# Kernel tuning notes

Measured on AMD Instinct MI355X. Metric: run time of the kernel, lower is better.

## Reference

```python
import jax, jax.numpy as jnp
import numpy as np

EMBED_DIM = 256
NUM_HEADS = 8
HEAD_DIM = EMBED_DIM // NUM_HEADS
SCALE = HEAD_DIM ** -0.5  # note: scale uses head_dim even though attention is over full D
EPS = 1e-12  # torch F.normalize eps


def setup_inputs() -> dict:
    key = jax.random.key(0)
    k1, k2, k3 = jax.random.split(key, 3)
    B, Nq, Nk, D = 4, 4096, 4096, EMBED_DIM
    return {
        "query": jax.random.normal(k1, (B, Nq, D), dtype=jnp.float32),
        "key": jax.random.normal(k2, (B, Nk, D), dtype=jnp.float32),
        "value": jax.random.normal(k3, (B, Nk, D), dtype=jnp.float32),
    }


def _l2_normalize(x):
    # matches torch.nn.functional.normalize(x, dim=-1): x / max(||x||, eps)
    n = jnp.linalg.norm(x, axis=-1, keepdims=True)
    return x / jnp.maximum(n, EPS)


def reference(query, key, value):
    q = _l2_normalize(query)          # (B, Nq, D)
    k = _l2_normalize(key)            # (B, Nk, D)
    scores = jnp.einsum("bqd,bkd->bqk", q, k) * SCALE  # (B, Nq, Nk) cosine sims
    attn = jax.nn.softmax(scores, axis=-1)
    return jnp.einsum("bqk,bkd->bqd", attn, value)     # (B, Nq, D)
```

## Files before the change

### kernel.cpp

```cpp
#include <hip/hip_runtime.h>


#define NQ 4096
#define NK 4096
#define DIM 256
#define NROWS 16384
#define BM 128
#define BN 64
#define KSPLIT 2
#define NITER 32

typedef __attribute__((ext_vector_type(8))) short bf16x8;
typedef __attribute__((ext_vector_type(4))) float f32x4;
typedef __attribute__((ext_vector_type(16))) float f32x16;

__device__ __forceinline__ unsigned short f2bf(float f) {
  unsigned int u = __float_as_uint(f);
  u += 0x7fffu + ((u >> 16) & 1u);
  return (unsigned short)(u >> 16);
}

__device__ __forceinline__ void gload16(const void* g, void* l) {
  __builtin_amdgcn_global_load_lds(
      (const __attribute__((address_space(1))) unsigned int*)g,
      (__attribute__((address_space(3))) unsigned int*)l, 16, 0, 0);
}

__global__ __launch_bounds__(256) void prep_qk(
    const float* __restrict__ Q, const float* __restrict__ K,
    unsigned short* __restrict__ Qfm, unsigned short* __restrict__ Kfm)
{
  const int wave = threadIdx.x >> 6, lane = threadIdx.x & 63;
  const int r = blockIdx.x * 4 + wave;
  const bool isQ = r < NROWS;
  const int R = isQ ? r : r - NROWS;
  const float* src = (isQ ? Q : K) + (size_t)R * DIM + lane * 4;
  float4 v = *(const float4*)src;
  float ss = v.x*v.x + v.y*v.y + v.z*v.z + v.w*v.w;
  #pragma unroll
  for (int off = 1; off < 64; off <<= 1) ss += __shfl_xor(ss, off, 64);
  float scale = 1.0f / fmaxf(sqrtf(ss), 1e-12f);
  if (isQ) scale *= (0.17677669529663687f * 1.4426950408889634f);
  unsigned short b0 = f2bf(v.x*scale), b1 = f2bf(v.y*scale),
                 b2 = f2bf(v.z*scale), b3 = f2bf(v.w*scale);
  ushort4 o; o.x = b0; o.y = b1; o.z = b2; o.w = b3;
  if (isQ) {
    const int mb = R >> 4, m = R & 15;
    const int kg = lane >> 3, fl = m + 16 * ((lane >> 1) & 3), j0 = 4 * (lane & 1);
    *(ushort4*)(Qfm + ((size_t)(mb*8 + kg)*64 + fl)*8 + j0) = o;
  } else {
    const int kt = R >> 6, n = R & 63;
    const int c = lane >> 1, j0 = 4 * (lane & 1);
    *(ushort4*)(Kfm + ((size_t)(kt*32 + c)*64 + n)*8 + j0) = o;
  }
}

__global__ __launch_bounds__(256) void prep_v(
    const float* __restrict__ V, unsigned short* __restrict__ Vfm)
{
  const int NS = blockIdx.x;
  const int t = threadIdx.x;
  #pragma unroll
  for (int i = 0; i < 4; i++) {
    const int e = t + 256*i;
    const int nl = e >> 6;
    const int d  = (e & 63) * 4;
    float4 v = *(const float4*)(V + ((size_t)NS*16 + nl)*DIM + d);
    const int db = d >> 5;
    const int lane = (d & 31) + 32*((nl >> 3) & 1);
    const int j = nl & 7;
    size_t base = ((size_t)(NS*8 + db)*64 + lane)*8 + j;
    Vfm[base]      = f2bf(v.x);
    Vfm[base + 8]  = f2bf(v.y);
    Vfm[base + 16] = f2bf(v.z);
    Vfm[base + 24] = f2bf(v.w);
  }
}

__global__ __launch_bounds__(512, 2) void attn(
    const unsigned short* __restrict__ Qfm,
    const unsigned short* __restrict__ Kfm,
    const unsigned short* __restrict__ Vfm,
    float* __restrict__ Opart, float* __restrict__ lpart)
{
  __shared__ unsigned short Klds[64 * 256];
  __shared__ unsigned short Plds[128 * 64];

  const int tid = threadIdx.x, wave = tid >> 6, lane = tid & 63;
  const int blk = blockIdx.x;
  const int g = blk & 7, qt = blk >> 3;
  const int b = g >> 1, ks = g & 1;
  const int Rq0 = b*NQ + qt*BM;
  const int MB0 = Rq0 >> 4;
  const int n0base = b*NQ + ks*(NK/KSPLIT);
  const int mi = wave >> 1, ni = wave & 1;
  const int mi2 = wave >> 2, dh = wave & 3;

  bf16x8 qf[2][8];
  #pragma unroll
  for (int mt = 0; mt < 2; mt++) {
    const int mb = MB0 + mi*2 + mt;
    #pragma unroll
    for (int kg = 0; kg < 8; kg++)
      qf[mt][kg] = *(const bf16x8*)(Qfm + ((size_t)(mb*8 + kg)*64 + lane)*8);
  }

  f32x16 oacc[2][2] = {};
  float lacc[2][4] = {};

  auto stage = [&](int kt) {
    const int ktile = (n0base + kt*BN) >> 6;
    #pragma unroll
    for (int jj = 0; jj < 4; jj++) {
      const int c = wave*4 + jj;
      gload16(Kfm + ((size_t)(ktile*32 + c)*64 + lane)*8, Klds + (size_t)c*512);
    }
  };

  stage(0);

  for (int kt = 0; kt < NITER; kt++) {
    __syncthreads();

    f32x4 sacc[2][2] = {};
    #pragma unroll
    for (int kg = 0; kg < 8; kg++) {
      bf16x8 kf[2];
      #pragma unroll
      for (int nt = 0; nt < 2; nt++) {
        const int nrow = ni*32 + nt*16 + (lane & 15);
        const int c = kg*4 + (lane >> 4);
        kf[nt] = *(const bf16x8*)(Klds + ((size_t)(c*64 + nrow))*8);
      }
      #pragma unroll
      for (int mt = 0; mt < 2; mt++)
        #pragma unroll
        for (int nt = 0; nt < 2; nt++)
          sacc[mt][nt] = __builtin_amdgcn_mfma_f32_16x16x32_bf16(
              qf[mt][kg], kf[nt], sacc[mt][nt], 0, 0, 0);
    }

    #pragma unroll
    for (int mt = 0; mt < 2; mt++)
      #pragma unroll
      for (int nt = 0; nt < 2; nt++)
        #pragma unroll
        for (int r = 0; r < 4; r++) {
          float p = __builtin_amdgcn_exp2f(sacc[mt][nt][r]);
          lacc[mt][r] += p;
          const int m = mi*32 + mt*16 + 4*(lane >> 4) + r;
          const int n = ni*32 + nt*16 + (lane & 15);
          const int cc = (n >> 3) ^ (m & 7);
          Plds[m*64 + cc*8 + (n & 7)] = f2bf(p);
        }

    __syncthreads();

    if (kt + 1 < NITER) stage(kt + 1);

    const int NB0 = (n0base + kt*BN) >> 4;
    #pragma unroll
    for (int kstep = 0; kstep < 4; kstep++) {
      bf16x8 pf[2], vf[2];
      #pragma unroll
      for (int mt2 = 0; mt2 < 2; mt2++) {
        const int m = mi2*64 + mt2*32 + (lane & 31);
        const int c2 = kstep*2 + (lane >> 5);
        pf[mt2] = *(const bf16x8*)(Plds + m*64 + ((c2 ^ (m & 7)) * 8));
      }
      #pragma unroll
      for (int dt = 0; dt < 2; dt++) {
        const int db = dh*2 + dt;
        vf[dt] = *(const bf16x8*)(Vfm + ((size_t)((NB0 + kstep)*8 + db)*64 + lane)*8);
      }
      #pragma unroll
      for (int mt2 = 0; mt2 < 2; mt2++)
        #pragma unroll
        for (int dt = 0; dt < 2; dt++)
          oacc[mt2][dt] = __builtin_amdgcn_mfma_f32_32x32x16_bf16(
              pf[mt2], vf[dt], oacc[mt2][dt], 0, 0, 0);
    }
  }

  #pragma unroll
  for (int mt = 0; mt < 2; mt++)
    #pragma unroll
    for (int r = 0; r < 4; r++) {
      float s = lacc[mt][r];
      s += __shfl_xor(s, 1, 64); s += __shfl_xor(s, 2, 64);
      s += __shfl_xor(s, 4, 64); s += __shfl_xor(s, 8, 64);
      if ((lane & 15) == 0) {
        const int m = mi*32 + mt*16 + 4*(lane >> 4) + r;
        lpart[(size_t)(ks*2 + ni)*NROWS + Rq0 + m] = s;
      }
    }

  #pragma unroll
  for (int mt2 = 0; mt2 < 2; mt2++)
    #pragma unroll
    for (int dt = 0; dt < 2; dt++)
      #pragma unroll
      for (int reg = 0; reg < 16; reg++) {
        const int m = mi2*64 + mt2*32 + 4*(lane >> 5) + (reg & 3) + 8*(reg >> 2);
        const int d = dh*64 + dt*32 + (lane & 31);
        Opart[((size_t)(ks*NROWS + Rq0 + m))*DIM + d] = oacc[mt2][dt][reg];
      }
}

__global__ __launch_bounds__(256) void combine(
    const float* __restrict__ Opart, const float* __restrict__ lpart,
    float* __restrict__ out)
{
  const size_t idx = (size_t)blockIdx.x*256 + threadIdx.x;
  const size_t e = idx*4;
  const int R = (int)(e >> 8);
  float4 a = *(const float4*)(Opart + e);
  float4 c = *(const float4*)(Opart + (size_t)NROWS*DIM + e);
  float ls = lpart[R] + lpart[NROWS + R] + lpart[2*NROWS + R] + lpart[3*NROWS + R];
  float inv = 1.0f / ls;
  float4 o;
  o.x = (a.x + c.x)*inv; o.y = (a.y + c.y)*inv;
  o.z = (a.z + c.z)*inv; o.w = (a.w + c.w)*inv;
  *(float4*)(out + e) = o;
}

extern "C" void kernel_launch(void* const* d_in, const int* in_sizes, int n_in,
                              void* d_out, int out_size, void* d_ws, size_t ws_size,
                              hipStream_t stream) {
  const float* Q = (const float*)d_in[0];
  const float* K = (const float*)d_in[1];
  const float* V = (const float*)d_in[2];
  char* ws = (char*)d_ws;
  unsigned short* Qfm = (unsigned short*)(ws);
  unsigned short* Kfm = (unsigned short*)(ws + 8388608);
  unsigned short* Vfm = (unsigned short*)(ws + 16777216);
  float* Opart = (float*)(ws + 25165824);
  float* lpart = (float*)(ws + 58720256);

  prep_qk<<<8192, 256, 0, stream>>>(Q, K, Qfm, Kfm);
  prep_v<<<1024, 256, 0, stream>>>(V, Vfm);
  attn<<<256, 512, 0, stream>>>(Qfm, Kfm, Vfm, Opart, lpart);
  combine<<<4096, 256, 0, stream>>>(Opart, lpart, (float*)d_out);
}
```

Before: 214.4 us.

## Halve attention tile to 64 rows, fuse prep kernels, transpose S via swapped MFMA

Merges the Q/K and V prep kernels into one launch and stages V through LDS so the transposed fragment layout is written as vector stores. The attention kernel drops from 128-row, 512-thread blocks to 64-row, 256-thread blocks, doubling the grid to 512 blocks. It swaps the MFMA operand order so score tiles come out transposed, which lets P be packed two bf16 per word and written to a padded LDS buffer as 8-byte stores. Q is now read row-major with no shuffle layout. The smaller tile should improve occupancy and shrink the P write cost, but each block now reloads K for fewer query rows, doubling total K traffic.

```diff
diff --git a/kernel.cpp b/kernel.cpp
--- a/kernel.cpp
+++ b/kernel.cpp
@@ -2,13 +2,13 @@
 
 
 #define NQ 4096
-#define NK 4096
 #define DIM 256
 #define NROWS 16384
-#define BM 128
+#define BM 64
 #define BN 64
 #define KSPLIT 2
 #define NITER 32
+#define PSTRIDE 68
 
 typedef __attribute__((ext_vector_type(8))) short bf16x8;
 typedef __attribute__((ext_vector_type(4))) float f32x4;
@@ -20,100 +20,113 @@
   return (unsigned short)(u >> 16);
 }
 
+__device__ __forceinline__ unsigned int pack2bf(float a, float b) {
+  unsigned int ua = __float_as_uint(a) + 0x8000u;
+  unsigned int ub = __float_as_uint(b) + 0x8000u;
+  return __builtin_amdgcn_perm(ub, ua, 0x07060302u);
+}
+
 __device__ __forceinline__ void gload16(const void* g, void* l) {
   __builtin_amdgcn_global_load_lds(
       (const __attribute__((address_space(1))) unsigned int*)g,
       (__attribute__((address_space(3))) unsigned int*)l, 16, 0, 0);
 }
 
-__global__ __launch_bounds__(256) void prep_qk(
+__global__ __launch_bounds__(256) void prep(
     const float* __restrict__ Q, const float* __restrict__ K,
-    unsigned short* __restrict__ Qfm, unsigned short* __restrict__ Kfm)
+    const float* __restrict__ V,
+    unsigned short* __restrict__ Qrm, unsigned short* __restrict__ Kfm,
+    unsigned short* __restrict__ Vfm)
 {
-  const int wave = threadIdx.x >> 6, lane = threadIdx.x & 63;
-  const int r = blockIdx.x * 4 + wave;
-  const bool isQ = r < NROWS;
-  const int R = isQ ? r : r - NROWS;
-  const float* src = (isQ ? Q : K) + (size_t)R * DIM + lane * 4;
-  float4 v = *(const float4*)src;
-  float ss = v.x*v.x + v.y*v.y + v.z*v.z + v.w*v.w;
-  #pragma unroll
-  for (int off = 1; off < 64; off <<= 1) ss += __shfl_xor(ss, off, 64);
-  float scale = 1.0f / fmaxf(sqrtf(ss), 1e-12f);
-  if (isQ) scale *= (0.17677669529663687f * 1.4426950408889634f);
-  unsigned short b0 = f2bf(v.x*scale), b1 = f2bf(v.y*scale),
-                 b2 = f2bf(v.z*scale), b3 = f2bf(v.w*scale);
-  ushort4 o; o.x = b0; o.y = b1; o.z = b2; o.w = b3;
-  if (isQ) {
-    const int mb = R >> 4, m = R & 15;
-    const int kg = lane >> 3, fl = m + 16 * ((lane >> 1) & 3), j0 = 4 * (lane & 1);
-    *(ushort4*)(Qfm + ((size_t)(mb*8 + kg)*64 + fl)*8 + j0) = o;
+  __shared__ unsigned short vt[16 * 264];
+  const int blk = blockIdx.x, tid = threadIdx.x;
+  if (blk < 8192) {
+    const int wave = tid >> 6, lane = tid & 63;
+    const int r = blk * 4 + wave;
+    const bool isQ = r < NROWS;
+    const int R = isQ ? r : r - NROWS;
+    float4 v = *(const float4*)((isQ ? Q : K) + (size_t)R * DIM + lane * 4);
+    float ss = v.x*v.x + v.y*v.y + v.z*v.z + v.w*v.w;
+    #pragma unroll
+    for (int off = 1; off < 64; off <<= 1) ss += __shfl_xor(ss, off, 64);
+    float scale = 1.0f / fmaxf(sqrtf(ss), 1e-12f);
+    if (isQ) scale *= (0.17677669529663687f * 1.4426950408889634f);
+    ushort4 o;
+    o.x = f2bf(v.x*scale); o.y = f2bf(v.y*scale);
+    o.z = f2bf(v.z*scale); o.w = f2bf(v.w*scale);
+    if (isQ) {
+      *(ushort4*)(Qrm + (size_t)R * DIM + lane * 4) = o;
+    } else {
+      const int kt = R >> 6, n = R & 63;
+      const int c = lane >> 1, j0 = 4 * (lane & 1);
+      *(ushort4*)(Kfm + ((size_t)(kt*32 + c)*64 + n)*8 + j0) = o;
+    }
   } else {
-    const int kt = R >> 6, n = R & 63;
-    const int c = lane >> 1, j0 = 4 * (lane & 1);
-    *(ushort4*)(Kfm + ((size_t)(kt*32 + c)*64 + n)*8 + j0) = o;
-  }
-}
-
-__global__ __launch_bounds__(256) void prep_v(
-    const float* __restrict__ V, unsigned short* __restrict__ Vfm)
-{
-  const int NS = blockIdx.x;
-  const int t = threadIdx.x;
-  #pragma unroll
-  for (int i = 0; i < 4; i++) {
-    const int e = t + 256*i;
-    const int nl = e >> 6;
-    const int d  = (e & 63) * 4;
-    float4 v = *(const float4*)(V + ((size_t)NS*16 + nl)*DIM + d);
-    const int db = d >> 5;
-    const int lane = (d & 31) + 32*((nl >> 3) & 1);
-    const int j = nl & 7;
-    size_t base = ((size_t)(NS*8 + db)*64 + lane)*8 + j;
-    Vfm[base]      = f2bf(v.x);
-    Vfm[base + 8]  = f2bf(v.y);
-    Vfm[base + 16] = f2bf(v.z);
-    Vfm[base + 24] = f2bf(v.w);
-  }
-}
-
-__global__ __launch_bounds__(512, 2) void attn(
-    const unsigned short* __restrict__ Qfm,
+    const int NS = blk - 8192;
+    #pragma unroll
+    for (int i = 0; i < 4; i++) {
+      const int e = tid + 256*i;
+      const int nl = e >> 6, d = (e & 63) * 4;
+      float4 v = *(const float4*)(V + ((size_t)NS*16 + nl)*DIM + d);
+      ushort4 o;
+      o.x = f2bf(v.x); o.y = f2bf(v.y); o.z = f2bf(v.z); o.w = f2bf(v.w);
+      *(ushort4*)(vt + nl*264 + d) = o;
+    }
+    __syncthreads();
+    #pragma unroll
+    for (int i = 0; i < 2; i++) {
+      const int ch = tid + 256*i;
+      const int db = ch >> 6, ln = ch & 63;
+      const int row0 = (ln >> 5) * 8, dd = db*32 + (ln & 31);
+      ushort4 a, b;
+      a.x = vt[(row0+0)*264 + dd]; a.y = vt[(row0+1)*264 + dd];
+      a.z = vt[(row0+2)*264 + dd]; a.w = vt[(row0+3)*264 + dd];
+      b.x = vt[(row0+4)*264 + dd]; b.y = vt[(row0+5)*264 + dd];
+      b.z = vt[(row0+6)*264 + dd]; b.w = vt[(row0+7)*264 + dd];
+      size_t base = ((size_t)(NS*8 + db)*64 + ln)*8;
+      *(ushort4*)(Vfm + base)     = a;
+      *(ushort4*)(Vfm + base + 4) = b;
+    }
+  }
+}
+
+__global__ __launch_bounds__(256, 2) void attn(
+    const unsigned short* __restrict__ Qrm,
     const unsigned short* __restrict__ Kfm,
     const unsigned short* __restrict__ Vfm,
     float* __restrict__ Opart, float* __restrict__ lpart)
 {
-  __shared__ unsigned short Klds[64 * 256];
-  __shared__ unsigned short Plds[128 * 64];
+  __shared__ unsigned short Klds[32 * 64 * 8];
+  __shared__ unsigned short Plds[BM * PSTRIDE];
 
   const int tid = threadIdx.x, wave = tid >> 6, lane = tid & 63;
+  const int l15 = lane & 15, l4 = lane >> 4;
   const int blk = blockIdx.x;
   const int g = blk & 7, qt = blk >> 3;
   const int b = g >> 1, ks = g & 1;
   const int Rq0 = b*NQ + qt*BM;
-  const int MB0 = Rq0 >> 4;
-  const int n0base = b*NQ + ks*(NK/KSPLIT);
-  const int mi = wave >> 1, ni = wave & 1;
-  const int mi2 = wave >> 2, dh = wave & 3;
+  const int n0base = b*NQ + ks*(NQ/KSPLIT);
+  const int mi = wave & 1, ni = wave >> 1;
 
   bf16x8 qf[2][8];
   #pragma unroll
   for (int mt = 0; mt < 2; mt++) {
-    const int mb = MB0 + mi*2 + mt;
+    const unsigned short* qrow = Qrm + (size_t)(Rq0 + mi*32 + mt*16 + l15) * DIM + l4*8;
     #pragma unroll
     for (int kg = 0; kg < 8; kg++)
-      qf[mt][kg] = *(const bf16x8*)(Qfm + ((size_t)(mb*8 + kg)*64 + lane)*8);
+      qf[mt][kg] = *(const bf16x8*)(qrow + kg*32);
   }
 
   f32x16 oacc[2][2] = {};
-  float lacc[2][4] = {};
+  float lacc[2] = {};
 
   auto stage = [&](int kt) {
-    const int ktile = (n0base + kt*BN) >> 6;
+    const unsigned short* src = Kfm + (size_t)((n0base + kt*BN) >> 6) * (32*64*8);
     #pragma unroll
     for (int jj = 0; jj < 4; jj++) {
-      const int c = wave*4 + jj;
-      gload16(Kfm + ((size_t)(ktile*32 + c)*64 + lane)*8, Klds + (size_t)c*512);
+      const int c = wave*8 + jj*2;
+      gload16(src + (size_t)c*512 + lane*8,       Klds + (size_t)c*512);
+      gload16(src + (size_t)(c+1)*512 + lane*8,   Klds + (size_t)(c+1)*512);
     }
   };
 
@@ -128,31 +141,34 @@
       bf16x8 kf[2];
       #pragma unroll
       for (int nt = 0; nt < 2; nt++) {
-        const int nrow = ni*32 + nt*16 + (lane & 15);
-        const int c = kg*4 + (lane >> 4);
+        const int nrow = ni*32 + nt*16 + l15;
+        const int c = kg*4 + l4;
         kf[nt] = *(const bf16x8*)(Klds + ((size_t)(c*64 + nrow))*8);
       }
-      #pragma unroll
-      for (int mt = 0; mt < 2; mt++)
-        #pragma unroll
-        for (int nt = 0; nt < 2; nt++)
-          sacc[mt][nt] = __builtin_amdgcn_mfma_f32_16x16x32_bf16(
-              qf[mt][kg], kf[nt], sacc[mt][nt], 0, 0, 0);
-    }
-
-    #pragma unroll
-    for (int mt = 0; mt < 2; mt++)
       #pragma unroll
       for (int nt = 0; nt < 2; nt++)
         #pragma unroll
-        for (int r = 0; r < 4; r++) {
-          float p = __builtin_amdgcn_exp2f(sacc[mt][nt][r]);
-          lacc[mt][r] += p;
-          const int m = mi*32 + mt*16 + 4*(lane >> 4) + r;
-          const int n = ni*32 + nt*16 + (lane & 15);
-          const int cc = (n >> 3) ^ (m & 7);
-          Plds[m*64 + cc*8 + (n & 7)] = f2bf(p);
-        }
+        for (int mt = 0; mt < 2; mt++)
+          sacc[nt][mt] = __builtin_amdgcn_mfma_f32_16x16x32_bf16(
+              kf[nt], qf[mt][kg], sacc[nt][mt], 0, 0, 0);
+    }
+
+    #pragma unroll
+    for (int nt = 0; nt < 2; nt++)
+      #pragma unroll
+      for (int mt = 0; mt < 2; mt++) {
+        float p0 = __builtin_amdgcn_exp2f(sacc[nt][mt][0]);
+        float p1 = __builtin_amdgcn_exp2f(sacc[nt][mt][1]);
+        float p2 = __builtin_amdgcn_exp2f(sacc[nt][mt][2]);
+        float p3 = __builtin_amdgcn_exp2f(sacc[nt][mt][3]);
+        lacc[mt] += (p0 + p1) + (p2 + p3);
+        uint2 pk;
+        pk.x = pack2bf(p0, p1);
+        pk.y = pack2bf(p2, p3);
+        const int m = mi*32 + mt*16 + l15;
+        const int n = ni*32 + nt*16 + 4*l4;
+        *(uint2*)(Plds + m*PSTRIDE + n) = pk;
+      }
 
     __syncthreads();
 
@@ -163,14 +179,12 @@
     for (int kstep = 0; kstep < 4; kstep++) {
       bf16x8 pf[2], vf[2];
       #pragma unroll
-      for (int mt2 = 0; mt2 < 2; mt2++) {
-        const int m = mi2*64 + mt2*32 + (lane & 31);
-        const int c2 = kstep*2 + (lane >> 5);
-        pf[mt2] = *(const bf16x8*)(Plds + m*64 + ((c2 ^ (m & 7)) * 8));
-      }
+      for (int mt2 = 0; mt2 < 2; mt2++)
+        pf[mt2] = *(const bf16x8*)(Plds + (mt2*32 + (lane & 31))*PSTRIDE
+                                   + kstep*16 + 8*(lane >> 5));
       #pragma unroll
       for (int dt = 0; dt < 2; dt++) {
-        const int db = dh*2 + dt;
+        const int db = wave*2 + dt;
         vf[dt] = *(const bf16x8*)(Vfm + ((size_t)((NB0 + kstep)*8 + db)*64 + lane)*8);
       }
       #pragma unroll
@@ -183,17 +197,13 @@
   }
 
   #pragma unroll
-  for (int mt = 0; mt < 2; mt++)
-    #pragma unroll
-    for (int r = 0; r < 4; r++) {
-      float s = lacc[mt][r];
-      s += __shfl_xor(s, 1, 64); s += __shfl_xor(s, 2, 64);
-      s += __shfl_xor(s, 4, 64); s += __shfl_xor(s, 8, 64);
-      if ((lane & 15) == 0) {
-        const int m = mi*32 + mt*16 + 4*(lane >> 4) + r;
-        lpart[(size_t)(ks*2 + ni)*NROWS + Rq0 + m] = s;
-      }
-    }
+  for (int mt = 0; mt < 2; mt++) {
+    float s = lacc[mt];
+    s += __shfl_xor(s, 16, 64);
+    s += __shfl_xor(s, 32, 64);
+    if (l4 == 0)
+      lpart[(size_t)(ks*2 + ni)*NROWS + Rq0 + mi*32 + mt*16 + l15] = s;
+  }
 
   #pragma unroll
   for (int mt2 = 0; mt2 < 2; mt2++)
@@ -201,8 +211,8 @@
     for (int dt = 0; dt < 2; dt++)
       #pragma unroll
       for (int reg = 0; reg < 16; reg++) {
-        const int m = mi2*64 + mt2*32 + 4*(lane >> 5) + (reg & 3) + 8*(reg >> 2);
-        const int d = dh*64 + dt*32 + (lane & 31);
+        const int m = mt2*32 + 4*(lane >> 5) + (reg & 3) + 8*(reg >> 2);
+        const int d = wave*64 + dt*32 + (lane & 31);
         Opart[((size_t)(ks*NROWS + Rq0 + m))*DIM + d] = oacc[mt2][dt][reg];
       }
 }
@@ -231,14 +241,13 @@
   const float* K = (const float*)d_in[1];
   const float* V = (const float*)d_in[2];
   char* ws = (char*)d_ws;
-  unsigned short* Qfm = (unsigned short*)(ws);
+  unsigned short* Qrm = (unsigned short*)(ws);
   unsigned short* Kfm = (unsigned short*)(ws + 8388608);
   unsigned short* Vfm = (unsigned short*)(ws + 16777216);
   float* Opart = (float*)(ws + 25165824);
   float* lpart = (float*)(ws + 58720256);
 
-  prep_qk<<<8192, 256, 0, stream>>>(Q, K, Qfm, Kfm);
-  prep_v<<<1024, 256, 0, stream>>>(V, Vfm);
-  attn<<<256, 512, 0, stream>>>(Qfm, Kfm, Vfm, Opart, lpart);
+  prep<<<9216, 256, 0, stream>>>(Q, K, V, Qrm, Kfm, Vfm);
+  attn<<<512, 256, 0, stream>>>(Qrm, Kfm, Vfm, Opart, lpart);
   combine<<<4096, 256, 0, stream>>>(Opart, lpart, (float*)d_out);
 }
```

Result: faster. 180.9 us (-15.6%).
